# Kernel tuning notes

Hardware: AMD Instinct MI355X
Metric: run time of the kernel (lower is better)

The kernel has to match this reference:

```python
import jax, jax.numpy as jnp
import numpy as np

N_S, N_T, E, B = 100000, 100000, 2000000, 10000
F_XS, F_XT, F_E, F_U = 10, 5, 10, 10


def setup_inputs() -> dict:
    key = jax.random.key(0)
    ks = jax.random.split(key, 8)
    return {
        "x_s": jax.random.normal(ks[0], (N_S, F_XS), dtype=jnp.float32),
        "x_t": jax.random.normal(ks[1], (N_T, F_XT), dtype=jnp.float32),
        "edge_index": jax.random.randint(ks[2], (2, E), 0, N_S),
        "edge_attr": jax.random.normal(ks[3], (E, F_E), dtype=jnp.float32),
        "u": jax.random.normal(ks[4], (B, F_U), dtype=jnp.float32),
        "batch_e": jax.random.randint(ks[5], (E,), 0, B),
        "W1": jax.random.normal(ks[6], (F_XS + F_XT + F_E + F_U, F_E), dtype=jnp.float32) * (1.0 / np.sqrt(F_XS + F_XT + F_E + F_U)),
        "b1": jnp.zeros((F_E,), dtype=jnp.float32),
        "W2": jax.random.normal(ks[7], (F_E, F_E), dtype=jnp.float32) * (1.0 / np.sqrt(F_E)),
        "b2": jnp.zeros((F_E,), dtype=jnp.float32),
    }


def reference(x_s, x_t, edge_index, edge_attr, u, batch_e, W1, b1, W2, b2):
    src, tgt = edge_index[0], edge_index[1]
    # Gather + concat: [E, F_xs + F_xt + F_e + F_u]
    h = jnp.concatenate([x_s[src], x_t[tgt], edge_attr, u[batch_e]], axis=-1)
    h = jax.nn.leaky_relu(h @ W1 + b1, negative_slope=0.1)
    return h @ W2 + b2  # [E, F_e]
```

## Files before the change

kernel.cpp:

```cpp
#include <hip/hip_runtime.h>


#define F_XS 10
#define F_XT 5
#define F_E  10
#define F_U  10
#define F_IN 35

typedef float vf4 __attribute__((ext_vector_type(4)));
typedef float vf2 __attribute__((ext_vector_type(2)));

__global__ __launch_bounds__(256) void edge_model_kernel(
    const float* __restrict__ x_s,
    const float* __restrict__ x_t,
    const int*   __restrict__ edge_index,
    const float* __restrict__ edge_attr,
    const float* __restrict__ u,
    const int*   __restrict__ batch_e,
    const float* __restrict__ W1,
    const float* __restrict__ b1,
    const float* __restrict__ W2,
    const float* __restrict__ b2,
    float*       __restrict__ out,
    int E)
{
    const int e = blockIdx.x * blockDim.x + threadIdx.x;
    if (e >= E) return;

    const int src = __builtin_nontemporal_load(edge_index + e);
    const int tgt = __builtin_nontemporal_load(edge_index + E + e);
    const int be  = __builtin_nontemporal_load(batch_e + e);

    const float* ps = x_s + (long long)src * F_XS;
    vf4 s0 = *(const vf4*)(ps);
    vf4 s1 = *(const vf4*)(ps + 4);
    vf2 s2 = *(const vf2*)(ps + 8);

    const float* pt = x_t + (long long)tgt * F_XT;
    vf4 t0 = *(const vf4*)(pt);
    float t1 = pt[4];

    const float* pe = edge_attr + (long long)e * F_E;
    vf4 a0 = __builtin_nontemporal_load((const vf4*)(pe));
    vf4 a1 = __builtin_nontemporal_load((const vf4*)(pe + 4));
    vf2 a2 = __builtin_nontemporal_load((const vf2*)(pe + 8));

    const float* pu = u + (long long)be * F_U;
    vf4 u0 = *(const vf4*)(pu);
    vf4 u1 = *(const vf4*)(pu + 4);
    vf2 u2 = *(const vf2*)(pu + 8);

    float h[F_E];
    #pragma unroll
    for (int j = 0; j < F_E; ++j) h[j] = b1[j];

    {
        float seg[10] = {s0.x,s0.y,s0.z,s0.w, s1.x,s1.y,s1.z,s1.w, s2.x,s2.y};
        #pragma unroll
        for (int k = 0; k < 10; ++k) {
            #pragma unroll
            for (int j = 0; j < F_E; ++j) h[j] = fmaf(seg[k], W1[k * F_E + j], h[j]);
        }
    }
    {
        float seg[5] = {t0.x,t0.y,t0.z,t0.w, t1};
        #pragma unroll
        for (int k = 0; k < 5; ++k) {
            #pragma unroll
            for (int j = 0; j < F_E; ++j) h[j] = fmaf(seg[k], W1[(10 + k) * F_E + j], h[j]);
        }
    }
    {
        float seg[10] = {a0.x,a0.y,a0.z,a0.w, a1.x,a1.y,a1.z,a1.w, a2.x,a2.y};
        #pragma unroll
        for (int k = 0; k < 10; ++k) {
            #pragma unroll
            for (int j = 0; j < F_E; ++j) h[j] = fmaf(seg[k], W1[(15 + k) * F_E + j], h[j]);
        }
    }
    {
        float seg[10] = {u0.x,u0.y,u0.z,u0.w, u1.x,u1.y,u1.z,u1.w, u2.x,u2.y};
        #pragma unroll
        for (int k = 0; k < 10; ++k) {
            #pragma unroll
            for (int j = 0; j < F_E; ++j) h[j] = fmaf(seg[k], W1[(25 + k) * F_E + j], h[j]);
        }
    }

    #pragma unroll
    for (int j = 0; j < F_E; ++j) h[j] = (h[j] >= 0.0f) ? h[j] : 0.1f * h[j];

    float o[F_E];
    #pragma unroll
    for (int j = 0; j < F_E; ++j) o[j] = b2[j];
    #pragma unroll
    for (int k = 0; k < F_E; ++k) {
        const float a = h[k];
        #pragma unroll
        for (int j = 0; j < F_E; ++j) o[j] = fmaf(a, W2[k * F_E + j], o[j]);
    }

    float* po = out + (long long)e * F_E;
    vf4 w0; w0.x=o[0]; w0.y=o[1]; w0.z=o[2]; w0.w=o[3];
    vf4 w1; w1.x=o[4]; w1.y=o[5]; w1.z=o[6]; w1.w=o[7];
    vf2 w2; w2.x=o[8]; w2.y=o[9];
    *(vf4*)(po)     = w0;
    *(vf4*)(po + 4) = w1;
    *(vf2*)(po + 8) = w2;
}

extern "C" void kernel_launch(void* const* d_in, const int* in_sizes, int n_in,
                              void* d_out, int out_size, void* d_ws, size_t ws_size,
                              hipStream_t stream) {
    const float* x_s        = (const float*)d_in[0];
    const float* x_t        = (const float*)d_in[1];
    const int*   edge_index = (const int*)  d_in[2];
    const float* edge_attr  = (const float*)d_in[3];
    const float* u          = (const float*)d_in[4];
    const int*   batch_e    = (const int*)  d_in[5];
    const float* W1         = (const float*)d_in[6];
    const float* b1         = (const float*)d_in[7];
    const float* W2         = (const float*)d_in[8];
    const float* b2         = (const float*)d_in[9];
    float*       out        = (float*)d_out;

    const int E = in_sizes[5];
    const int block = 256;
    const int grid  = (E + block - 1) / block;

    edge_model_kernel<<<grid, block, 0, stream>>>(
        x_s, x_t, edge_index, edge_attr, u, batch_e, W1, b1, W2, b2, out, E);
}
```

Measured before the change: 244.2 us.

## Convert gathered node and global tables to fp16 in workspace before edge kernel

Adds a pre-pass kernel that converts x_s, x_t (padded to 6 halves per row) and u into fp16 copies in the workspace, and the edge kernel then gathers from these half-size tables. This is meant to cut the bytes moved by the random gathers, which dominate traffic. In exchange it adds an extra launch and a conversion pass over the tables on every call, and lowers input precision to fp16 before the matmul. A plain fp32 fallback kernel is kept for when the workspace is too small.

```diff
diff --git a/kernel.cpp b/kernel.cpp
--- a/kernel.cpp
+++ b/kernel.cpp
@@ -9,13 +9,37 @@
 
 typedef float vf4 __attribute__((ext_vector_type(4)));
 typedef float vf2 __attribute__((ext_vector_type(2)));
-
-__global__ __launch_bounds__(256) void edge_model_kernel(
-    const float* __restrict__ x_s,
-    const float* __restrict__ x_t,
+typedef _Float16 f16;
+
+__global__ __launch_bounds__(256) void convert_tables_kernel(
+    const float* __restrict__ xs, const float* __restrict__ xt, const float* __restrict__ uu,
+    f16* __restrict__ xs_h, f16* __restrict__ xt_h, f16* __restrict__ u_h,
+    int n_xs_elems, int n_u_elems, int n_t_rows)
+{
+    const int tid = blockIdx.x * blockDim.x + threadIdx.x;
+    if (tid < n_xs_elems) {
+        xs_h[tid] = (f16)xs[tid];
+    } else if (tid < n_xs_elems + n_u_elems) {
+        const int i = tid - n_xs_elems;
+        u_h[i] = (f16)uu[i];
+    } else {
+        const int r = tid - n_xs_elems - n_u_elems;
+        if (r < n_t_rows) {
+            const float* p = xt + (long long)r * F_XT;
+            f16* q = xt_h + (long long)r * 6;
+            #pragma unroll
+            for (int i = 0; i < 5; ++i) q[i] = (f16)p[i];
+            q[5] = (f16)0.f;
+        }
+    }
+}
+
+__global__ __launch_bounds__(256) void edge_model_f16tab_kernel(
+    const f16*   __restrict__ xs_h,
+    const f16*   __restrict__ xt_h,
     const int*   __restrict__ edge_index,
     const float* __restrict__ edge_attr,
-    const float* __restrict__ u,
+    const f16*   __restrict__ u_h,
     const int*   __restrict__ batch_e,
     const float* __restrict__ W1,
     const float* __restrict__ b1,
@@ -31,44 +55,30 @@
     const int tgt = __builtin_nontemporal_load(edge_index + E + e);
     const int be  = __builtin_nontemporal_load(batch_e + e);
 
-    const float* ps = x_s + (long long)src * F_XS;
-    vf4 s0 = *(const vf4*)(ps);
-    vf4 s1 = *(const vf4*)(ps + 4);
-    vf2 s2 = *(const vf2*)(ps + 8);
-
-    const float* pt = x_t + (long long)tgt * F_XT;
-    vf4 t0 = *(const vf4*)(pt);
-    float t1 = pt[4];
+    f16 s[10];  __builtin_memcpy(s, xs_h + (long long)src * 10, 20);
+    f16 t[8];   __builtin_memcpy(t, xt_h + (long long)tgt * 6, 16);
+    f16 uv[10]; __builtin_memcpy(uv, u_h + (long long)be * 10, 20);
 
     const float* pe = edge_attr + (long long)e * F_E;
     vf4 a0 = __builtin_nontemporal_load((const vf4*)(pe));
     vf4 a1 = __builtin_nontemporal_load((const vf4*)(pe + 4));
     vf2 a2 = __builtin_nontemporal_load((const vf2*)(pe + 8));
 
-    const float* pu = u + (long long)be * F_U;
-    vf4 u0 = *(const vf4*)(pu);
-    vf4 u1 = *(const vf4*)(pu + 4);
-    vf2 u2 = *(const vf2*)(pu + 8);
-
     float h[F_E];
     #pragma unroll
     for (int j = 0; j < F_E; ++j) h[j] = b1[j];
 
-    {
-        float seg[10] = {s0.x,s0.y,s0.z,s0.w, s1.x,s1.y,s1.z,s1.w, s2.x,s2.y};
-        #pragma unroll
-        for (int k = 0; k < 10; ++k) {
-            #pragma unroll
-            for (int j = 0; j < F_E; ++j) h[j] = fmaf(seg[k], W1[k * F_E + j], h[j]);
-        }
-    }
-    {
-        float seg[5] = {t0.x,t0.y,t0.z,t0.w, t1};
-        #pragma unroll
-        for (int k = 0; k < 5; ++k) {
-            #pragma unroll
-            for (int j = 0; j < F_E; ++j) h[j] = fmaf(seg[k], W1[(10 + k) * F_E + j], h[j]);
-        }
+    #pragma unroll
+    for (int k = 0; k < 10; ++k) {
+        const float a = (float)s[k];
+        #pragma unroll
+        for (int j = 0; j < F_E; ++j) h[j] = fmaf(a, W1[k * F_E + j], h[j]);
+    }
+    #pragma unroll
+    for (int k = 0; k < 5; ++k) {
+        const float a = (float)t[k];
+        #pragma unroll
+        for (int j = 0; j < F_E; ++j) h[j] = fmaf(a, W1[(10 + k) * F_E + j], h[j]);
     }
     {
         float seg[10] = {a0.x,a0.y,a0.z,a0.w, a1.x,a1.y,a1.z,a1.w, a2.x,a2.y};
@@ -78,13 +88,11 @@
             for (int j = 0; j < F_E; ++j) h[j] = fmaf(seg[k], W1[(15 + k) * F_E + j], h[j]);
         }
     }
-    {
-        float seg[10] = {u0.x,u0.y,u0.z,u0.w, u1.x,u1.y,u1.z,u1.w, u2.x,u2.y};
-        #pragma unroll
-        for (int k = 0; k < 10; ++k) {
-            #pragma unroll
-            for (int j = 0; j < F_E; ++j) h[j] = fmaf(seg[k], W1[(25 + k) * F_E + j], h[j]);
-        }
+    #pragma unroll
+    for (int k = 0; k < 10; ++k) {
+        const float a = (float)uv[k];
+        #pragma unroll
+        for (int j = 0; j < F_E; ++j) h[j] = fmaf(a, W1[(25 + k) * F_E + j], h[j]);
     }
 
     #pragma unroll
@@ -100,6 +108,62 @@
         for (int j = 0; j < F_E; ++j) o[j] = fmaf(a, W2[k * F_E + j], o[j]);
     }
 
+    float* po = out + (long long)e * F_E;
+    vf4 w0; w0.x=o[0]; w0.y=o[1]; w0.z=o[2]; w0.w=o[3];
+    vf4 w1; w1.x=o[4]; w1.y=o[5]; w1.z=o[6]; w1.w=o[7];
+    vf2 w2; w2.x=o[8]; w2.y=o[9];
+    *(vf4*)(po)     = w0;
+    *(vf4*)(po + 4) = w1;
+    *(vf2*)(po + 8) = w2;
+}
+
+__global__ __launch_bounds__(256) void edge_model_f32_kernel(
+    const float* __restrict__ x_s, const float* __restrict__ x_t,
+    const int*   __restrict__ edge_index, const float* __restrict__ edge_attr,
+    const float* __restrict__ u, const int* __restrict__ batch_e,
+    const float* __restrict__ W1, const float* __restrict__ b1,
+    const float* __restrict__ W2, const float* __restrict__ b2,
+    float* __restrict__ out, int E)
+{
+    const int e = blockIdx.x * blockDim.x + threadIdx.x;
+    if (e >= E) return;
+    const int src = __builtin_nontemporal_load(edge_index + e);
+    const int tgt = __builtin_nontemporal_load(edge_index + E + e);
+    const int be  = __builtin_nontemporal_load(batch_e + e);
+
+    float in[F_IN];
+    __builtin_memcpy(in,      x_s + (long long)src * F_XS, 40);
+    __builtin_memcpy(in + 10, x_t + (long long)tgt * F_XT, 20);
+    const float* pe = edge_attr + (long long)e * F_E;
+    vf4 a0 = __builtin_nontemporal_load((const vf4*)(pe));
+    vf4 a1 = __builtin_nontemporal_load((const vf4*)(pe + 4));
+    vf2 a2 = __builtin_nontemporal_load((const vf2*)(pe + 8));
+    in[15]=a0.x; in[16]=a0.y; in[17]=a0.z; in[18]=a0.w;
+    in[19]=a1.x; in[20]=a1.y; in[21]=a1.z; in[22]=a1.w;
+    in[23]=a2.x; in[24]=a2.y;
+    __builtin_memcpy(in + 25, u + (long long)be * F_U, 40);
+
+    float h[F_E];
+    #pragma unroll
+    for (int j = 0; j < F_E; ++j) h[j] = b1[j];
+    #pragma unroll
+    for (int k = 0; k < F_IN; ++k) {
+        const float a = in[k];
+        #pragma unroll
+        for (int j = 0; j < F_E; ++j) h[j] = fmaf(a, W1[k * F_E + j], h[j]);
+    }
+    #pragma unroll
+    for (int j = 0; j < F_E; ++j) h[j] = (h[j] >= 0.0f) ? h[j] : 0.1f * h[j];
+
+    float o[F_E];
+    #pragma unroll
+    for (int j = 0; j < F_E; ++j) o[j] = b2[j];
+    #pragma unroll
+    for (int k = 0; k < F_E; ++k) {
+        const float a = h[k];
+        #pragma unroll
+        for (int j = 0; j < F_E; ++j) o[j] = fmaf(a, W2[k * F_E + j], o[j]);
+    }
     float* po = out + (long long)e * F_E;
     vf4 w0; w0.x=o[0]; w0.y=o[1]; w0.z=o[2]; w0.w=o[3];
     vf4 w1; w1.x=o[4]; w1.y=o[5]; w1.z=o[6]; w1.w=o[7];
@@ -124,10 +188,36 @@
     const float* b2         = (const float*)d_in[9];
     float*       out        = (float*)d_out;
 
-    const int E = in_sizes[5];
+    const int E   = in_sizes[5];
+    const int N_S = in_sizes[0] / F_XS;
+    const int N_T = in_sizes[1] / F_XT;
+    const int Bn  = in_sizes[4] / F_U;
+
+    const size_t xs_bytes = (size_t)N_S * 10 * sizeof(f16);
+    const size_t xs_off   = 0;
+    const size_t xt_off   = (xs_off + xs_bytes + 15) & ~(size_t)15;
+    const size_t xt_bytes = (size_t)N_T * 6 * sizeof(f16) + 16;
+    const size_t u_off    = (xt_off + xt_bytes + 15) & ~(size_t)15;
+    const size_t u_bytes  = (size_t)Bn * 10 * sizeof(f16);
+    const size_t need     = u_off + u_bytes;
+
     const int block = 256;
-    const int grid  = (E + block - 1) / block;
-
-    edge_model_kernel<<<grid, block, 0, stream>>>(
-        x_s, x_t, edge_index, edge_attr, u, batch_e, W1, b1, W2, b2, out, E);
-}
+    const int grid_e = (E + block - 1) / block;
+
+    if (ws_size >= need) {
+        f16* xs_h = (f16*)((char*)d_ws + xs_off);
+        f16* xt_h = (f16*)((char*)d_ws + xt_off);
+        f16* u_h  = (f16*)((char*)d_ws + u_off);
+
+        const int n_xs = N_S * 10, n_u = Bn * 10;
+        const int conv_threads = n_xs + n_u + N_T;
+        convert_tables_kernel<<<(conv_threads + block - 1) / block, block, 0, stream>>>(
+            x_s, x_t, u, xs_h, xt_h, u_h, n_xs, n_u, N_T);
+
+        edge_model_f16tab_kernel<<<grid_e, block, 0, stream>>>(
+            xs_h, xt_h, edge_index, edge_attr, u_h, batch_e, W1, b1, W2, b2, out, E);
+    } else {
+        edge_model_f32_kernel<<<grid_e, block, 0, stream>>>(
+            x_s, x_t, edge_index, edge_attr, u, batch_e, W1, b1, W2, b2, out, E);
+    }
+}
```

Result: faster. 239.0 us (-2.1%).
